# Kernel tuning notes

Measured on AMD Instinct MI355X. Metric: run time of the kernel, lower is better.

Reference implementation:

```python
import jax, jax.numpy as jnp
import numpy as np

D_MODEL = 1024
N_HEAD = 16
N_HEAD_MOE = 8
N_EXPERTS = 8
TOP_N = 2
CAP_FACTOR = 1.25
THRESHOLD = 0.2
BAL_COEF = 0.01
Z_COEF = 0.001
B, S = 8, 1024


def setup_inputs() -> dict:
    key = jax.random.key(0)
    ks = jax.random.split(key, 12)
    d, E = D_MODEL, N_EXPERTS
    w = lambda k, shape: jax.random.normal(k, shape, jnp.float32) * 0.02
    return {
        "x": jax.random.normal(ks[0], (B, S, d), jnp.float32),
        "Wq": w(ks[1], (d, d)), "Wk": w(ks[2], (d, d)), "Wv": w(ks[3], (d, d)), "Wo": w(ks[4], (d, d)),
        "bq": jnp.zeros((d,), jnp.float32), "bk": jnp.zeros((d,), jnp.float32),
        "bv": jnp.zeros((d,), jnp.float32), "bo": jnp.zeros((d,), jnp.float32),
        "ln1_g": jnp.ones((d,), jnp.float32), "ln1_b": jnp.zeros((d,), jnp.float32),
        "ln2_g": jnp.ones((d,), jnp.float32), "ln2_b": jnp.zeros((d,), jnp.float32),
        "gate_W": w(ks[5], (d, E)),
        "eWq": w(ks[6], (E, d, d)), "eWk": w(ks[7], (E, d, d)),
        "eWv": w(ks[8], (E, d, d)), "eWo": w(ks[9], (E, d, d)),
    }


def _layernorm(x, g, b, eps=1e-5):
    mu = jnp.mean(x, -1, keepdims=True)
    var = jnp.var(x, -1, keepdims=True)
    return (x - mu) * jax.lax.rsqrt(var + eps) * g + b


def _mha(x, Wq, Wk, Wv, bq, bk, bv, Wo, bo):
    b, s, d = x.shape
    h, hd = N_HEAD, d // N_HEAD
    q = (x @ Wq + bq).reshape(b, s, h, hd)
    k = (x @ Wk + bk).reshape(b, s, h, hd)
    v = (x @ Wv + bv).reshape(b, s, h, hd)
    att = jax.nn.softmax(jnp.einsum('bqhd,bkhd->bhqk', q, k) * (hd ** -0.5), axis=-1)
    o = jnp.einsum('bhqk,bkhd->bqhd', att, v).reshape(b, s, d)
    return o @ Wo + bo


def _moe(x, gate_W, eWq, eWk, eWv, eWo):
    # ST-MoE style top-n routing with capacity dropping; experts are self-attention blocks.
    b, s, d = x.shape
    E = N_EXPERTS
    C = int(S * TOP_N * CAP_FACTOR / E)  # per-expert capacity (per batch row)
    logits = x @ gate_W                      # [b,s,E]
    z_loss = jnp.mean(jnp.square(jax.nn.logsumexp(logits, axis=-1)))
    probs = jax.nn.softmax(logits, axis=-1)
    gates, idxs = jax.lax.top_k(probs, TOP_N)  # [b,s,TOP_N]
    # load-balance loss: E * sum_e (top-1 dispatch fraction) * (mean router prob)
    f = jnp.mean(jax.nn.one_hot(idxs[..., 0], E, dtype=x.dtype), axis=(0, 1))
    P = jnp.mean(probs, axis=(0, 1))
    balance_loss = E * jnp.sum(f * P)

    bb = jnp.broadcast_to(jnp.arange(b)[:, None], (b, s))
    counts = jnp.zeros((b, E), jnp.int32)
    expert_in = jnp.zeros((E, b, C, d), x.dtype)
    slots = []
    for k in range(TOP_N):  # small fixed loop over routing slots
        e_idx = idxs[..., k]
        g = gates[..., k]
        keep_thr = (g > THRESHOLD) if k > 0 else jnp.ones(g.shape, dtype=bool)
        oh = jax.nn.one_hot(e_idx, E, dtype=jnp.int32) * keep_thr[..., None].astype(jnp.int32)
        # exclusive running position within each (batch, expert) buffer
        pos_all = jnp.cumsum(oh, axis=1) - oh + counts[:, None, :]
        pos = jnp.take_along_axis(pos_all, e_idx[..., None], axis=2)[..., 0]
        counts = counts + jnp.sum(oh, axis=1)
        keep = keep_thr & (pos < C)
        p = jnp.clip(pos, 0, C - 1)
        expert_in = expert_in.at[e_idx, bb, p].add(x * keep[..., None].astype(x.dtype))
        slots.append((e_idx, p, keep, g))

    # each expert: multi-head self-attention over its C capacity slots
    h, hd = N_HEAD_MOE, d // N_HEAD_MOE
    q = jnp.einsum('ebcd,edf->ebcf', expert_in, eWq).reshape(E, b, C, h, hd)
    kk = jnp.einsum('ebcd,edf->ebcf', expert_in, eWk).reshape(E, b, C, h, hd)
    v = jnp.einsum('ebcd,edf->ebcf', expert_in, eWv).reshape(E, b, C, h, hd)
    att = jax.nn.softmax(jnp.einsum('ebqhd,ebkhd->ebhqk', q, kk) * (hd ** -0.5), axis=-1)
    o = jnp.einsum('ebhqk,ebkhd->ebqhd', att, v).reshape(E, b, C, d)
    expert_out = jnp.einsum('ebcd,edf->ebcf', o, eWo)

    # combine: gather each token's slot output, weighted by its gate
    y = jnp.zeros_like(x)
    for e_idx, p, keep, g in slots:
        y = y + expert_out[e_idx, bb, p] * (g * keep.astype(x.dtype))[..., None]
    bal = BAL_COEF * balance_loss
    zl = Z_COEF * z_loss
    return y, bal + zl, bal, zl


def reference(x, Wq, Wk, Wv, Wo, bq, bk, bv, bo, ln1_g, ln1_b, ln2_g, ln2_b,
              gate_W, eWq, eWk, eWv, eWo):
    attn = _mha(x, Wq, Wk, Wv, bq, bk, bv, Wo, bo)
    x1 = _layernorm(x + attn, ln1_g, ln1_b)
    moe_out, aux, bal, zl = _moe(x1, gate_W, eWq, eWk, eWv, eWo)
    out = _layernorm(x1 + moe_out, ln2_g, ln2_b)
    return (out, aux, bal, zl)
```

## Files before the change

### kernel.cpp

```cpp
#include <hip/hip_runtime.h>
#include <hip/hip_bf16.h>
#include <math.h>

#define DM    1024
#define NH1   16
#define HDIM1 64
#define NH2   8
#define HDIM2 128
#define NE    8
#define CAPE  320
#define BATCH 8
#define SEQ   1024
#define NTOK  (BATCH*SEQ)
#define OUTN  ((long)NTOK*DM)

typedef short bf16x8 __attribute__((ext_vector_type(8)));
typedef float f32x4  __attribute__((ext_vector_type(4)));

__device__ __forceinline__ unsigned short f2bf(float f) {
    __hip_bfloat16 h = __float2bfloat16(f);
    return *reinterpret_cast<unsigned short*>(&h);
}
__device__ __forceinline__ float bf2f(unsigned short u) {
    unsigned int x = ((unsigned int)u) << 16;
    return __builtin_bit_cast(float, x);
}

__device__ __forceinline__ void async16(const void* g, void* lds) {
    __builtin_amdgcn_global_load_lds(
        (const __attribute__((address_space(1))) unsigned int*)g,
        (__attribute__((address_space(3))) unsigned int*)lds, 16, 0, 0);
}

__device__ __forceinline__ void gemm_core(
    const unsigned short* __restrict__ A, const unsigned short* __restrict__ Bt,
    int m0, int n0, int K, short* ldsA, short* ldsB, f32x4 (&acc)[4][4])
{
    const int t    = threadIdx.x;
    const int lane = t & 63, w = t >> 6;
    const int wr = w >> 1, wc = w & 1;
    const int lq = lane >> 4, lm = lane & 15;
    const int srow = w*16 + (lane >> 2);
    const int skc  = (lane & 3) * 8;
    for (int kb = 0; kb < K; kb += 32) {
        #pragma unroll
        for (int p = 0; p < 2; ++p) {
            async16(A  + (size_t)(m0 + srow + p*64)*K + kb + skc,
                    &ldsA[(w*16 + p*64)*32]);
            async16(Bt + (size_t)(n0 + srow + p*64)*K + kb + skc,
                    &ldsB[(w*16 + p*64)*32]);
        }
        __syncthreads();
        bf16x8 aF[4], bF[4];
        #pragma unroll
        for (int i = 0; i < 4; ++i)
            aF[i] = *(const bf16x8*)&ldsA[(wr*64 + i*16 + lm)*32 + lq*8];
        #pragma unroll
        for (int j = 0; j < 4; ++j)
            bF[j] = *(const bf16x8*)&ldsB[(wc*64 + j*16 + lm)*32 + lq*8];
        #pragma unroll
        for (int i = 0; i < 4; ++i)
            #pragma unroll
            for (int j = 0; j < 4; ++j)
                acc[i][j] = __builtin_amdgcn_mfma_f32_16x16x32_bf16(aF[i], bF[j], acc[i][j], 0, 0, 0);
        __syncthreads();
    }
}

__global__ __launch_bounds__(256) void gemm_bt_f32(
    const unsigned short* __restrict__ A, const unsigned short* __restrict__ Bt,
    const float* __restrict__ bias, float* __restrict__ C, int N, int K)
{
    __shared__ short ldsA[128*32];
    __shared__ short ldsB[128*32];
    const int lane = threadIdx.x & 63, w = threadIdx.x >> 6;
    const int wr = w >> 1, wc = w & 1;
    const int lq = lane >> 4, lm = lane & 15;
    const int m0 = blockIdx.y * 128, n0 = blockIdx.x * 128;
    f32x4 acc[4][4];
    #pragma unroll
    for (int i = 0; i < 4; ++i)
        #pragma unroll
        for (int j = 0; j < 4; ++j) acc[i][j] = (f32x4){0.f,0.f,0.f,0.f};
    gemm_core(A, Bt, m0, n0, K, ldsA, ldsB, acc);
    #pragma unroll
    for (int j = 0; j < 4; ++j) {
        const int gcol = n0 + wc*64 + j*16 + lm;
        const float badd = bias ? bias[gcol] : 0.f;
        #pragma unroll
        for (int i = 0; i < 4; ++i) {
            const int grow = m0 + wr*64 + i*16 + lq*4;
            #pragma unroll
            for (int r = 0; r < 4; ++r)
                C[(size_t)(grow + r)*N + gcol] = acc[i][j][r] + badd;
        }
    }
}

__global__ __launch_bounds__(256) void gemm_qkv(
    const unsigned short* __restrict__ A, const unsigned short* __restrict__ Bt,
    const float* __restrict__ bq, const float* __restrict__ bk, const float* __restrict__ bv,
    unsigned short* __restrict__ C)
{
    __shared__ short ldsA[128*32];
    __shared__ short ldsB[128*32];
    const int lane = threadIdx.x & 63, w = threadIdx.x >> 6;
    const int wr = w >> 1, wc = w & 1;
    const int lq = lane >> 4, lm = lane & 15;
    const int m0 = blockIdx.y * 128, n0g = blockIdx.x * 128;
    const int buf = n0g >> 10;
    const float* bias = (buf == 0) ? bq : (buf == 1) ? bk : bv;
    unsigned short* Cb = C + (size_t)buf * OUTN;
    f32x4 acc[4][4];
    #pragma unroll
    for (int i = 0; i < 4; ++i)
        #pragma unroll
        for (int j = 0; j < 4; ++j) acc[i][j] = (f32x4){0.f,0.f,0.f,0.f};
    gemm_core(A, Bt, m0, n0g, DM, ldsA, ldsB, acc);
    #pragma unroll
    for (int j = 0; j < 4; ++j) {
        const int gcol = (n0g & 1023) + wc*64 + j*16 + lm;
        const float badd = bias[gcol];
        #pragma unroll
        for (int i = 0; i < 4; ++i) {
            const int grow = m0 + wr*64 + i*16 + lq*4;
            #pragma unroll
            for (int r = 0; r < 4; ++r)
                Cb[(size_t)(grow + r)*DM + gcol] = f2bf(acc[i][j][r] + badd);
        }
    }
}

__global__ __launch_bounds__(256) void gemm_eqkv_gather(
    const unsigned short* __restrict__ X1b, const int* __restrict__ slotmap,
    const unsigned short* __restrict__ zbuf,
    const unsigned short* __restrict__ eWTq, const unsigned short* __restrict__ eWTk,
    const unsigned short* __restrict__ eWTv,
    unsigned short* __restrict__ Cq, unsigned short* __restrict__ Ck,
    unsigned short* __restrict__ Cv, int ebase)
{
    __shared__ short ldsA[128*32];
    __shared__ short ldsB[128*32];
    const int lane = threadIdx.x & 63, w = threadIdx.x >> 6;
    const int wr = w >> 1, wc = w & 1;
    const int lq = lane >> 4, lm = lane & 15;
    const int z = blockIdx.z;
    const int eloc = blockIdx.y / 20;
    const unsigned short* Bt =
        ((z == 0) ? eWTq : (z == 1) ? eWTk : eWTv) + (size_t)(ebase + eloc) * (1024l*1024l);
    unsigned short* C = (z == 0) ? Cq : (z == 1) ? Ck : Cv;
    const int m0 = blockIdx.y * 128, n0 = blockIdx.x * 128;
    const int srow = w*16 + (lane >> 2);
    const int skc  = (lane & 3) * 8;
    const int sbase = ebase * (BATCH*CAPE);
    const int t0 = slotmap[sbase + m0 + srow];
    const int t1 = slotmap[sbase + m0 + srow + 64];
    const unsigned short* a0 = (t0 >= 0) ? X1b + (size_t)t0 * DM : zbuf;
    const unsigned short* a1 = (t1 >= 0) ? X1b + (size_t)t1 * DM : zbuf;
    f32x4 acc[4][4];
    #pragma unroll
    for (int i = 0; i < 4; ++i)
        #pragma unroll
        for (int j = 0; j < 4; ++j) acc[i][j] = (f32x4){0.f,0.f,0.f,0.f};
    for (int kb = 0; kb < DM; kb += 32) {
        async16(a0 + kb + skc, &ldsA[(w*16)*32]);
        async16(a1 + kb + skc, &ldsA[(w*16 + 64)*32]);
        async16(Bt + (size_t)(n0 + srow)*DM + kb + skc,      &ldsB[(w*16)*32]);
        async16(Bt + (size_t)(n0 + srow + 64)*DM + kb + skc, &ldsB[(w*16 + 64)*32]);
        __syncthreads();
        bf16x8 aF[4], bF[4];
        #pragma unroll
        for (int i = 0; i < 4; ++i)
            aF[i] = *(const bf16x8*)&ldsA[(wr*64 + i*16 + lm)*32 + lq*8];
        #pragma unroll
        for (int j = 0; j < 4; ++j)
            bF[j] = *(const bf16x8*)&ldsB[(wc*64 + j*16 + lm)*32 + lq*8];
        #pragma unroll
        for (int i = 0; i < 4; ++i)
            #pragma unroll
            for (int j = 0; j < 4; ++j)
                acc[i][j] = __builtin_amdgcn_mfma_f32_16x16x32_bf16(aF[i], bF[j], acc[i][j], 0, 0, 0);
        __syncthreads();
    }
    #pragma unroll
    for (int j = 0; j < 4; ++j) {
        const int gcol = n0 + wc*64 + j*16 + lm;
        #pragma unroll
        for (int i = 0; i < 4; ++i) {
            const int grow = m0 + wr*64 + i*16 + lq*4;
            #pragma unroll
            for (int r = 0; r < 4; ++r)
                C[(size_t)(grow + r)*DM + gcol] = f2bf(acc[i][j][r]);
        }
    }
}

__global__ __launch_bounds__(256) void gemm_eout(
    const unsigned short* __restrict__ A, const unsigned short* __restrict__ eWTo,
    unsigned short* __restrict__ C, int ebase)
{
    __shared__ short ldsA[128*32];
    __shared__ short ldsB[128*32];
    const int lane = threadIdx.x & 63, w = threadIdx.x >> 6;
    const int wr = w >> 1, wc = w & 1;
    const int lq = lane >> 4, lm = lane & 15;
    const int eloc = blockIdx.y / 20;
    const unsigned short* Bt = eWTo + (size_t)(ebase + eloc) * (1024l*1024l);
    const int m0 = blockIdx.y * 128, n0 = blockIdx.x * 128;
    f32x4 acc[4][4];
    #pragma unroll
    for (int i = 0; i < 4; ++i)
        #pragma unroll
        for (int j = 0; j < 4; ++j) acc[i][j] = (f32x4){0.f,0.f,0.f,0.f};
    gemm_core(A, Bt, m0, n0, DM, ldsA, ldsB, acc);
    #pragma unroll
    for (int j = 0; j < 4; ++j) {
        const int gcol = n0 + wc*64 + j*16 + lm;
        #pragma unroll
        for (int i = 0; i < 4; ++i) {
            const int grow = m0 + wr*64 + i*16 + lq*4;
            #pragma unroll
            for (int r = 0; r < 4; ++r)
                C[(size_t)(grow + r)*DM + gcol] = f2bf(acc[i][j][r]);
        }
    }
}

template<int HD, int NS>
__global__ __launch_bounds__(256) void flash_mfma(
    const unsigned short* __restrict__ Q, const unsigned short* __restrict__ K,
    const unsigned short* __restrict__ V, unsigned short* __restrict__ O,
    int rows, float scale)
{
    constexpr int KT = 64;
    constexpr int PADQ = HD + 8;
    constexpr int NKT = HD / 32;
    constexpr int NDT = HD / 16;
    constexpr int CG  = HD / 8;
    constexpr int RPR = 256 / CG;
    constexpr int NP  = KT / RPR;
    constexpr int PST = 76;
    __shared__ __align__(16) unsigned short ks[KT * PADQ];
    __shared__ __align__(16) unsigned short vt[HD * KT];
    __shared__ __align__(16) unsigned short pP[4][16 * PST];
    const int t = threadIdx.x, lane = t & 63, w = t >> 6;
    const int lm = lane & 15, quad = lane >> 4;
    const int q0 = blockIdx.x * (64 * NS);
    const long base = (long)blockIdx.z * rows * DM + (long)blockIdx.y * HD;
    const int srow = t / CG, scg = t % CG;

    bf16x8 aQ[NS][NKT];
    #pragma unroll
    for (int s = 0; s < NS; ++s) {
        if (s) __syncthreads();
        #pragma unroll
        for (int r = 0; r < 64 / RPR; ++r) {
            int row = srow + r * RPR;
            *(bf16x8*)&ks[row * PADQ + scg * 8] =
                *(const bf16x8*)&Q[base + (long)(q0 + s * 64 + row) * DM + scg * 8];
        }
        __syncthreads();
        #pragma unroll
        for (int kk = 0; kk < NKT; ++kk)
            aQ[s][kk] = *(const bf16x8*)&ks[(w * 16 + lm) * PADQ + kk * 32 + quad * 8];
    }

    float m4[NS][4], l4[NS][4];
    f32x4 aco[NS][NDT];
    #pragma unroll
    for (int s = 0; s < NS; ++s) {
        #pragma unroll
        for (int r = 0; r < 4; ++r) { m4[s][r] = -1e30f; l4[s][r] = 0.f; }
        #pragma unroll
        for (int d = 0; d < NDT; ++d) aco[s][d] = (f32x4){0.f,0.f,0.f,0.f};
    }

    bf16x8 kr[NP], vr[NP];
    #pragma unroll
    for (int r = 0; r < NP; ++r) {
        int row = srow + r * RPR;
        kr[r] = *(const bf16x8*)&K[base + (long)row * DM + scg * 8];
        vr[r] = *(const bf16x8*)&V[base + (long)row * DM + scg * 8];
    }

    for (int k0 = 0; k0 < rows; k0 += KT) {
        __syncthreads();
        #pragma unroll
        for (int r = 0; r < NP; ++r) {
            int row = srow + r * RPR;
            *(bf16x8*)&ks[row * PADQ + scg * 8] = kr[r];
            #pragma unroll
            for (int u = 0; u < 8; ++u) {
                int d = scg * 8 + u;
                vt[d * KT + ((((row >> 3) ^ (d >> 3) ^ d) & 7)) * 8 + (row & 7)] = ((short*)&vr[r])[u];
            }
        }
        __syncthreads();
        if (k0 + KT < rows) {
            #pragma unroll
            for (int r = 0; r < NP; ++r) {
                int row = srow + r * RPR;
                kr[r] = *(const bf16x8*)&K[base + (long)(k0 + KT + row) * DM + scg * 8];
                vr[r] = *(const bf16x8*)&V[base + (long)(k0 + KT + row) * DM + scg * 8];
            }
        }
        #pragma unroll
        for (int s = 0; s < NS; ++s) {
            f32x4 sc[4];
            #pragma unroll
            for (int n = 0; n < 4; ++n) {
                f32x4 c = (f32x4){0.f,0.f,0.f,0.f};
                #pragma unroll
                for (int kk = 0; kk < NKT; ++kk) {
                    bf16x8 bK = *(const bf16x8*)&ks[(n * 16 + lm) * PADQ + kk * 32 + quad * 8];
                    c = __builtin_amdgcn_mfma_f32_16x16x32_bf16(aQ[s][kk], bK, c, 0, 0, 0);
                }
                #pragma unroll
                for (int r = 0; r < 4; ++r) c[r] *= scale;
                sc[n] = c;
            }
            float alpha[4];
            #pragma unroll
            for (int r = 0; r < 4; ++r) {
                float mx = fmaxf(fmaxf(sc[0][r], sc[1][r]), fmaxf(sc[2][r], sc[3][r]));
                #pragma unroll
                for (int off = 1; off < 16; off <<= 1)
                    mx = fmaxf(mx, __shfl_xor(mx, off, 64));
                float mnew = fmaxf(m4[s][r], mx);
                alpha[r] = __expf(m4[s][r] - mnew);
                m4[s][r] = mnew;
                float sum = 0.f;
                #pragma unroll
                for (int n = 0; n < 4; ++n) {
                    float p = __expf(sc[n][r] - mnew);
                    sc[n][r] = p; sum += p;
                }
                #pragma unroll
                for (int off = 1; off < 16; off <<= 1)
                    sum += __shfl_xor(sum, off, 64);
                l4[s][r] = l4[s][r] * alpha[r] + sum;
            }
            #pragma unroll
            for (int n = 0; n < 4; ++n)
                #pragma unroll
                for (int r = 0; r < 4; ++r)
                    pP[w][(quad * 4 + r) * PST + n * 16 + lm] = f2bf(sc[n][r]);
            #pragma unroll
            for (int d = 0; d < NDT; ++d)
                #pragma unroll
                for (int r = 0; r < 4; ++r) aco[s][d][r] *= alpha[r];
            #pragma unroll
            for (int d = 0; d < NDT; ++d) {
                #pragma unroll
                for (int kk = 0; kk < 2; ++kk) {
                    bf16x8 aP = *(const bf16x8*)&pP[w][lm * PST + kk * 32 + quad * 8];
                    int dd = d * 16 + lm;
                    int jb = kk * 4 + quad;
                    bf16x8 bV = *(const bf16x8*)&vt[dd * KT + (((jb ^ (dd >> 3) ^ dd) & 7) * 8)];
                    aco[s][d] = __builtin_amdgcn_mfma_f32_16x16x32_bf16(aP, bV, aco[s][d], 0, 0, 0);
                }
            }
        }
    }
    #pragma unroll
    for (int s = 0; s < NS; ++s)
        #pragma unroll
        for (int r = 0; r < 4; ++r) {
            float inv = 1.f / l4[s][r];
            #pragma unroll
            for (int d = 0; d < NDT; ++d)
                O[base + (long)(q0 + s * 64 + w * 16 + quad * 4 + r) * DM + d * 16 + lm] =
                    f2bf(aco[s][d][r] * inv);
        }
}

__global__ __launch_bounds__(256) void transpose_bf16(
    const float* __restrict__ src, unsigned short* __restrict__ dst)
{
    __shared__ float tile[32][33];
    const long mb = (long)blockIdx.z * (1024l*1024l);
    const int tx = threadIdx.x & 31, ty = threadIdx.x >> 5;
    const int r0 = blockIdx.y * 32, c0 = blockIdx.x * 32;
    #pragma unroll
    for (int rr = ty; rr < 32; rr += 8)
        tile[rr][tx] = src[mb + (long)(r0+rr)*1024 + c0 + tx];
    __syncthreads();
    #pragma unroll
    for (int rr = ty; rr < 32; rr += 8)
        dst[mb + (long)(c0+rr)*1024 + r0 + tx] = f2bf(tile[tx][rr]);
}

__global__ __launch_bounds__(256) void convert_bf16(
    const float* __restrict__ src, unsigned short* __restrict__ dst, long n)
{
    long i = ((long)blockIdx.x*256 + threadIdx.x)*4;
    if (i >= n) return;
    float4 v = *(const float4*)&src[i];
    ushort4 o = { f2bf(v.x), f2bf(v.y), f2bf(v.z), f2bf(v.w) };
    *(ushort4*)&dst[i] = o;
}

__global__ __launch_bounds__(256) void ln_residual(
    const float* __restrict__ X, const float* __restrict__ R,
    const float* __restrict__ gam, const float* __restrict__ bet,
    float* __restrict__ Yf, unsigned short* __restrict__ Yb)
{
    const long row = blockIdx.x;
    const int t = threadIdx.x;
    float4 xv = *(const float4*)&X[row*DM + t*4];
    float4 rv = *(const float4*)&R[row*DM + t*4];
    float v0=xv.x+rv.x, v1=xv.y+rv.y, v2=xv.z+rv.z, v3=xv.w+rv.w;
    float s  = v0+v1+v2+v3;
    float s2 = v0*v0+v1*v1+v2*v2+v3*v3;
    #pragma unroll
    for (int off = 32; off > 0; off >>= 1) {
        s  += __shfl_down(s,  off, 64);
        s2 += __shfl_down(s2, off, 64);
    }
    __shared__ float red[8];
    __shared__ float mv[2];
    const int wid = t >> 6;
    if ((t & 63) == 0) { red[wid] = s; red[4+wid] = s2; }
    __syncthreads();
    if (t == 0) {
        float S  = red[0]+red[1]+red[2]+red[3];
        float S2 = red[4]+red[5]+red[6]+red[7];
        float mean = S * (1.f/DM);
        float var  = S2 * (1.f/DM) - mean*mean;
        mv[0] = mean; mv[1] = rsqrtf(var + 1e-5f);
    }
    __syncthreads();
    float mean = mv[0], inv = mv[1];
    float4 g4 = *(const float4*)&gam[t*4];
    float4 b4 = *(const float4*)&bet[t*4];
    float4 o4;
    o4.x = (v0-mean)*inv*g4.x + b4.x;
    o4.y = (v1-mean)*inv*g4.y + b4.y;
    o4.z = (v2-mean)*inv*g4.z + b4.z;
    o4.w = (v3-mean)*inv*g4.w + b4.w;
    *(float4*)&Yf[row*DM + t*4] = o4;
    ushort4 ub = { f2bf(o4.x), f2bf(o4.y), f2bf(o4.z), f2bf(o4.w) };
    *(ushort4*)&Yb[row*DM + t*4] = ub;
}

__global__ __launch_bounds__(256) void accum_chunk(
    float* __restrict__ out, const unsigned short* __restrict__ Eout,
    const int* __restrict__ e1, const int* __restrict__ pos1,
    const int* __restrict__ keep1, const float* __restrict__ g1,
    const int* __restrict__ e2, const int* __restrict__ pos2,
    const int* __restrict__ keep2, const float* __restrict__ g2,
    int ebase)
{
    const long row = blockIdx.x;
    const int b = (int)(row >> 10);
    const int t = threadIdx.x;
    const int E1 = e1[row] - ebase;
    const int E2 = e2[row] - ebase;
    const bool h1 = (E1 >= 0) && (E1 < 4) && (keep1[row] != 0);
    const bool h2 = (E2 >= 0) && (E2 < 4) && (keep2[row] != 0);
    if (!h1 && !h2) return;
    float4 acc = *(const float4*)&out[row*DM + t*4];
    if (h1) {
        const float w1 = g1[row];
        ushort4 u = *(const ushort4*)&Eout[((size_t)(E1*BATCH + b)*CAPE + pos1[row])*DM + t*4];
        acc.x += w1*bf2f(u.x); acc.y += w1*bf2f(u.y);
        acc.z += w1*bf2f(u.z); acc.w += w1*bf2f(u.w);
    }
    if (h2) {
        const float w2 = g2[row];
        ushort4 u = *(const ushort4*)&Eout[((size_t)(E2*BATCH + b)*CAPE + pos2[row])*DM + t*4];
        acc.x += w2*bf2f(u.x); acc.y += w2*bf2f(u.y);
        acc.z += w2*bf2f(u.z); acc.w += w2*bf2f(u.w);
    }
    *(float4*)&out[row*DM + t*4] = acc;
}

__global__ __launch_bounds__(256) void ln_inplace(
    float* __restrict__ Y, const float* __restrict__ gam, const float* __restrict__ bet)
{
    const long row = blockIdx.x;
    const int t = threadIdx.x;
    float4 xv = *(const float4*)&Y[row*DM + t*4];
    float v0=xv.x, v1=xv.y, v2=xv.z, v3=xv.w;
    float s  = v0+v1+v2+v3;
    float s2 = v0*v0+v1*v1+v2*v2+v3*v3;
    #pragma unroll
    for (int off = 32; off > 0; off >>= 1) {
        s  += __shfl_down(s,  off, 64);
        s2 += __shfl_down(s2, off, 64);
    }
    __shared__ float red[8];
    __shared__ float mv[2];
    const int wid = t >> 6;
    if ((t & 63) == 0) { red[wid] = s; red[4+wid] = s2; }
    __syncthreads();
    if (t == 0) {
        float S  = red[0]+red[1]+red[2]+red[3];
        float S2 = red[4]+red[5]+red[6]+red[7];
        float mean = S * (1.f/DM);
        float var  = S2 * (1.f/DM) - mean*mean;
        mv[0] = mean; mv[1] = rsqrtf(var + 1e-5f);
    }
    __syncthreads();
    float mean = mv[0], inv = mv[1];
    float4 g4 = *(const float4*)&gam[t*4];
    float4 b4 = *(const float4*)&bet[t*4];
    float4 o4;
    o4.x = (v0-mean)*inv*g4.x + b4.x;
    o4.y = (v1-mean)*inv*g4.y + b4.y;
    o4.z = (v2-mean)*inv*g4.z + b4.z;
    o4.w = (v3-mean)*inv*g4.w + b4.w;
    *(float4*)&Y[row*DM + t*4] = o4;
}

__global__ __launch_bounds__(256) void gate_kernel(
    const float* __restrict__ X1, const float* __restrict__ gW,
    int* __restrict__ e1, int* __restrict__ e2,
    float* __restrict__ g1, float* __restrict__ g2,
    float* __restrict__ accum)
{
    const int t = threadIdx.x, l = t & 63, w = t >> 6;
    const int gwave = blockIdx.x * 4 + w;
    float zacc = 0.f, pacc[8], facc[8];
    #pragma unroll
    for (int e = 0; e < 8; ++e) { pacc[e] = 0.f; facc[e] = 0.f; }

    for (int tok = gwave; tok < NTOK; tok += 2048) {
        const float* xr = X1 + (long)tok*DM;
        float part[8];
        #pragma unroll
        for (int e = 0; e < 8; ++e) part[e] = 0.f;
        #pragma unroll
        for (int pass = 0; pass < 4; ++pass) {
            const int i0 = pass*256 + l*4;
            float4 xv = *(const float4*)&xr[i0];
            const float xs[4] = {xv.x, xv.y, xv.z, xv.w};
            #pragma unroll
            for (int u = 0; u < 4; ++u) {
                float4 w0 = *(const float4*)&gW[(i0+u)*8];
                float4 w1 = *(const float4*)&gW[(i0+u)*8+4];
                part[0]+=xs[u]*w0.x; part[1]+=xs[u]*w0.y; part[2]+=xs[u]*w0.z; part[3]+=xs[u]*w0.w;
                part[4]+=xs[u]*w1.x; part[5]+=xs[u]*w1.y; part[6]+=xs[u]*w1.z; part[7]+=xs[u]*w1.w;
            }
        }
        #pragma unroll
        for (int e = 0; e < 8; ++e) {
            float v = part[e];
            #pragma unroll
            for (int off = 32; off > 0; off >>= 1) v += __shfl_down(v, off, 64);
            part[e] = v;
        }
        if (l == 0) {
            float mx = part[0];
            #pragma unroll
            for (int e = 1; e < 8; ++e) mx = fmaxf(mx, part[e]);
            float p[8]; float sum = 0.f;
            #pragma unroll
            for (int e = 0; e < 8; ++e) { p[e] = __expf(part[e]-mx); sum += p[e]; }
            float lse = mx + __logf(sum);
            float isum = 1.f/sum;
            #pragma unroll
            for (int e = 0; e < 8; ++e) { p[e] *= isum; pacc[e] += p[e]; }
            int b1 = 0;
            #pragma unroll
            for (int e = 1; e < 8; ++e) if (p[e] > p[b1]) b1 = e;
            int b2 = (b1 == 0) ? 1 : 0;
            #pragma unroll
            for (int e = 0; e < 8; ++e) if (e != b1 && e != b2 && p[e] > p[b2]) b2 = e;
            e1[tok] = b1; e2[tok] = b2; g1[tok] = p[b1]; g2[tok] = p[b2];
            zacc += lse*lse;
            facc[b1] += 1.f;
        }
    }
    __shared__ float red[4][17];
    if (l == 0) {
        red[w][0] = zacc;
        #pragma unroll
        for (int e = 0; e < 8; ++e) { red[w][1+e] = pacc[e]; red[w][9+e] = facc[e]; }
    }
    __syncthreads();
    if (t < 17)
        atomicAdd(&accum[t], red[0][t] + red[1][t] + red[2][t] + red[3][t]);
}

__global__ __launch_bounds__(64) void route_scan(
    const int* __restrict__ e1, const int* __restrict__ e2,
    const float* __restrict__ g2,
    int* __restrict__ pos1, int* __restrict__ keep1,
    int* __restrict__ pos2, int* __restrict__ keep2,
    int* __restrict__ slotmap)
{
    const int b = blockIdx.x;
    const int l = threadIdx.x;
    __shared__ int cnt[8];
    if (l < 8) cnt[l] = 0;
    __syncthreads();
    for (int slot = 0; slot < 2; ++slot) {
        const int* eArr = slot ? e2 : e1;
        for (int c = 0; c < SEQ/64; ++c) {
            const int tk = b*SEQ + c*64 + l;
            const int e = eArr[tk];
            const bool valid = slot ? (g2[tk] > 0.2f) : true;
            unsigned long long mymask = 0ull; int addmine = 0;
            #pragma unroll
            for (int ee = 0; ee < 8; ++ee) {
                unsigned long long bm = __ballot(valid && (e == ee));
                if (e == ee) mymask = bm;
                if (l == ee) addmine = (int)__popcll(bm);
            }
            const int p  = cnt[e] + (int)__popcll(mymask & ((1ull << l) - 1ull));
            const int kp = (valid && p < CAPE) ? 1 : 0;
            const int pc = p < CAPE ? p : (CAPE-1);
            if (slot == 0) { pos1[tk] = pc; keep1[tk] = kp; }
            else           { pos2[tk] = pc; keep2[tk] = kp; }
            if (kp) slotmap[(e*BATCH + b)*CAPE + pc] = tk;
            __syncthreads();
            if (l < 8) cnt[l] += addmine;
            __syncthreads();
        }
    }
}

__global__ void finalize_loss(const float* __restrict__ accum, float* __restrict__ out)
{
    float z = accum[0] * (1.0f/NTOK);
    float s = 0.f;
    for (int e = 0; e < 8; ++e)
        s += (accum[1+e] * (1.0f/NTOK)) * (accum[9+e] * (1.0f/NTOK));
    float bal = 0.01f * 8.0f * s;
    float zl  = 0.001f * z;
    out[OUTN]   = bal + zl;
    out[OUTN+1] = bal;
    out[OUTN+2] = zl;
}

extern "C" void kernel_launch(void* const* d_in, const int* in_sizes, int n_in,
                              void* d_out, int out_size, void* d_ws, size_t ws_size,
                              hipStream_t stream)
{
    (void)in_sizes; (void)n_in; (void)out_size; (void)ws_size;
    const float* x    = (const float*)d_in[0];
    const float* Wq   = (const float*)d_in[1];
    const float* Wk   = (const float*)d_in[2];
    const float* Wv   = (const float*)d_in[3];
    const float* Wo   = (const float*)d_in[4];
    const float* bq   = (const float*)d_in[5];
    const float* bk   = (const float*)d_in[6];
    const float* bv   = (const float*)d_in[7];
    const float* bo   = (const float*)d_in[8];
    const float* ln1g = (const float*)d_in[9];
    const float* ln1b = (const float*)d_in[10];
    const float* ln2g = (const float*)d_in[11];
    const float* ln2b = (const float*)d_in[12];
    const float* gW   = (const float*)d_in[13];
    const float* eWq  = (const float*)d_in[14];
    const float* eWk  = (const float*)d_in[15];
    const float* eWv  = (const float*)d_in[16];
    const float* eWo  = (const float*)d_in[17];
    float* out = (float*)d_out;

    char* ws = (char*)d_ws;
    const size_t MB = 1048576;
    const long MATE = 1024l*1024l;
    unsigned short* WTq  = (unsigned short*)(ws);
    unsigned short* WTk  = WTq + 1*MATE;
    unsigned short* WTv  = WTq + 2*MATE;
    unsigned short* WTo  = WTq + 3*MATE;
    unsigned short* eWTq = WTq + 4*MATE;
    unsigned short* eWTk = WTq + 12*MATE;
    unsigned short* eWTv = WTq + 20*MATE;
    unsigned short* eWTo = WTq + 28*MATE;
    int*   e1i   = (int*)(ws + 72*MB);
    int*   e2i   = e1i + NTOK;
    int*   pos1  = e1i + 2*NTOK;
    int*   pos2  = e1i + 3*NTOK;
    int*   keep1 = e1i + 4*NTOK;
    int*   keep2 = e1i + 5*NTOK;
    int*   slotmap = e1i + 6*NTOK;
    float* g1f   = (float*)(e1i + 6*NTOK + NE*BATCH*CAPE);
    float* g2f   = g1f + NTOK;
    float* accum = g2f + NTOK;
    unsigned short* zbuf = (unsigned short*)(ws + 73*MB);
    unsigned short* xb  = (unsigned short*)(ws + 74*MB);
    unsigned short* x1b = (unsigned short*)(ws + 74*MB);
    unsigned short* ob  = (unsigned short*)(ws + 90*MB);
    unsigned short* Qb  = (unsigned short*)(ws + 106*MB);
    float* Pf = (float*)(ws + 106*MB);
    unsigned short* eqb = (unsigned short*)(ws + 90*MB);
    unsigned short* ekb = (unsigned short*)(ws + 110*MB);
    unsigned short* evb = (unsigned short*)(ws + 130*MB);
    unsigned short* eob = (unsigned short*)(ws + 150*MB);
    unsigned short* eoc = eqb;

    dim3 blk(256);
    dim3 tgrid(32, 32, 1), tgrid8(32, 32, 8);

    transpose_bf16<<<tgrid,  blk, 0, stream>>>(Wq,  WTq);
    transpose_bf16<<<tgrid,  blk, 0, stream>>>(Wk,  WTk);
    transpose_bf16<<<tgrid,  blk, 0, stream>>>(Wv,  WTv);
    transpose_bf16<<<tgrid,  blk, 0, stream>>>(Wo,  WTo);
    transpose_bf16<<<tgrid8, blk, 0, stream>>>(eWq, eWTq);
    transpose_bf16<<<tgrid8, blk, 0, stream>>>(eWk, eWTk);
    transpose_bf16<<<tgrid8, blk, 0, stream>>>(eWv, eWTv);
    transpose_bf16<<<tgrid8, blk, 0, stream>>>(eWo, eWTo);
    convert_bf16<<<NTOK, blk, 0, stream>>>(x, xb, OUTN);

    gemm_qkv<<<dim3(3*DM/128, NTOK/128), blk, 0, stream>>>(xb, WTq, bq, bk, bv, Qb);
    flash_mfma<HDIM1,1><<<dim3(SEQ/64, NH1, BATCH), blk, 0, stream>>>(
        Qb, Qb + OUTN, Qb + 2*OUTN, ob, SEQ, 0.125f);
    gemm_bt_f32<<<dim3(DM/128, NTOK/128), blk, 0, stream>>>(ob, WTo, bo, Pf, DM, DM);
    ln_residual<<<NTOK, blk, 0, stream>>>(x, Pf, ln1g, ln1b, out, x1b);

    hipMemsetAsync(accum, 0, 17*sizeof(float), stream);
    hipMemsetAsync(slotmap, 0xFF, NE*BATCH*CAPE*sizeof(int), stream);
    hipMemsetAsync(zbuf, 0, 4096, stream);
    gate_kernel<<<512, blk, 0, stream>>>(out, gW, e1i, e2i, g1f, g2f, accum);
    route_scan<<<BATCH, dim3(64), 0, stream>>>(e1i, e2i, g2f, pos1, keep1, pos2, keep2, slotmap);

    for (int c = 0; c < 2; ++c) {
        const int ebase = c*4;
        gemm_eqkv_gather<<<dim3(DM/128, 4*BATCH*CAPE/128, 3), blk, 0, stream>>>(
            x1b, slotmap, zbuf, eWTq, eWTk, eWTv, eqb, ekb, evb, ebase);
        flash_mfma<HDIM2,1><<<dim3(CAPE/64, NH2, 4*BATCH), blk, 0, stream>>>(
            eqb, ekb, evb, eob, CAPE, 0.088388347648318447f);
        gemm_eout<<<dim3(DM/128, 4*BATCH*CAPE/128), blk, 0, stream>>>(
            eob, eWTo, eoc, ebase);
        accum_chunk<<<NTOK, blk, 0, stream>>>(out, eoc, e1i, pos1, keep1, g1f,
                                              e2i, pos2, keep2, g2f, ebase);
    }

    ln_inplace<<<NTOK, blk, 0, stream>>>(out, ln2g, ln2b);
    finalize_loss<<<1, 1, 0, stream>>>(accum, out);
}
```

Before: 917.0 us.

## Add lazy softmax rescale, batch weight transposes, and process all experts per chunk

The flash attention loop now skips the exp-rescale of the running max and the accumulator unless some row's new max exceeds the old one by more than 8, which saves exp and multiply work on most tiles. The eight weight-transpose launches are merged into two. When the workspace is large enough, all eight experts are processed in one chunk instead of two, halving the launches of the expert kernels and the accumulation pass. The lazy rescale lets probabilities exceed 1 (up to e^8) before bf16 rounding, and the chunk size now depends on the workspace size.

New measurement: 935.4 us. +2.0%, slower.

```diff
diff --git a/kernel.cpp b/kernel.cpp
--- a/kernel.cpp
+++ b/kernel.cpp
@@ -319,36 +319,56 @@
                 for (int r = 0; r < 4; ++r) c[r] *= scale;
                 sc[n] = c;
             }
-            float alpha[4];
+            float mxv[4];
+            bool need = false;
             #pragma unroll
             for (int r = 0; r < 4; ++r) {
                 float mx = fmaxf(fmaxf(sc[0][r], sc[1][r]), fmaxf(sc[2][r], sc[3][r]));
                 #pragma unroll
                 for (int off = 1; off < 16; off <<= 1)
                     mx = fmaxf(mx, __shfl_xor(mx, off, 64));
-                float mnew = fmaxf(m4[s][r], mx);
-                alpha[r] = __expf(m4[s][r] - mnew);
-                m4[s][r] = mnew;
-                float sum = 0.f;
+                mxv[r] = mx;
+                need = need || (mx > m4[s][r] + 8.f);
+            }
+            if (__any(need ? 1 : 0)) {
                 #pragma unroll
-                for (int n = 0; n < 4; ++n) {
-                    float p = __expf(sc[n][r] - mnew);
-                    sc[n][r] = p; sum += p;
+                for (int r = 0; r < 4; ++r) {
+                    float mnew = fmaxf(m4[s][r], mxv[r]);
+                    float alpha = __expf(m4[s][r] - mnew);
+                    m4[s][r] = mnew;
+                    float sum = 0.f;
+                    #pragma unroll
+                    for (int n = 0; n < 4; ++n) {
+                        float p = __expf(sc[n][r] - mnew);
+                        sc[n][r] = p; sum += p;
+                    }
+                    #pragma unroll
+                    for (int off = 1; off < 16; off <<= 1)
+                        sum += __shfl_xor(sum, off, 64);
+                    l4[s][r] = l4[s][r] * alpha + sum;
+                    #pragma unroll
+                    for (int d = 0; d < NDT; ++d) aco[s][d][r] *= alpha;
                 }
+            } else {
                 #pragma unroll
-                for (int off = 1; off < 16; off <<= 1)
-                    sum += __shfl_xor(sum, off, 64);
-                l4[s][r] = l4[s][r] * alpha[r] + sum;
+                for (int r = 0; r < 4; ++r) {
+                    float sum = 0.f;
+                    #pragma unroll
+                    for (int n = 0; n < 4; ++n) {
+                        float p = __expf(sc[n][r] - m4[s][r]);
+                        sc[n][r] = p; sum += p;
+                    }
+                    #pragma unroll
+                    for (int off = 1; off < 16; off <<= 1)
+                        sum += __shfl_xor(sum, off, 64);
+                    l4[s][r] += sum;
+                }
             }
             #pragma unroll
             for (int n = 0; n < 4; ++n)
                 #pragma unroll
                 for (int r = 0; r < 4; ++r)
                     pP[w][(quad * 4 + r) * PST + n * 16 + lm] = f2bf(sc[n][r]);
-            #pragma unroll
-            for (int d = 0; d < NDT; ++d)
-                #pragma unroll
-                for (int r = 0; r < 4; ++r) aco[s][d][r] *= alpha[r];
             #pragma unroll
             for (int d = 0; d < NDT; ++d) {
                 #pragma unroll
@@ -374,20 +394,26 @@
         }
 }
 
-__global__ __launch_bounds__(256) void transpose_bf16(
-    const float* __restrict__ src, unsigned short* __restrict__ dst)
+__global__ __launch_bounds__(256) void transpose_many(
+    const float* __restrict__ s0, const float* __restrict__ s1,
+    const float* __restrict__ s2, const float* __restrict__ s3,
+    unsigned short* __restrict__ dst, int per)
 {
     __shared__ float tile[32][33];
-    const long mb = (long)blockIdx.z * (1024l*1024l);
+    const int z = blockIdx.z;
+    const int m = z / per;
+    const float* src = ((m == 0) ? s0 : (m == 1) ? s1 : (m == 2) ? s2 : s3)
+                       + (long)(z % per) * (1024l*1024l);
+    unsigned short* d = dst + (long)z * (1024l*1024l);
     const int tx = threadIdx.x & 31, ty = threadIdx.x >> 5;
     const int r0 = blockIdx.y * 32, c0 = blockIdx.x * 32;
     #pragma unroll
     for (int rr = ty; rr < 32; rr += 8)
-        tile[rr][tx] = src[mb + (long)(r0+rr)*1024 + c0 + tx];
+        tile[rr][tx] = src[(long)(r0+rr)*1024 + c0 + tx];
     __syncthreads();
     #pragma unroll
     for (int rr = ty; rr < 32; rr += 8)
-        dst[mb + (long)(c0+rr)*1024 + r0 + tx] = f2bf(tile[tx][rr]);
+        d[(long)(c0+rr)*1024 + r0 + tx] = f2bf(tile[tx][rr]);
 }
 
 __global__ __launch_bounds__(256) void convert_bf16(
@@ -449,15 +475,15 @@
     const int* __restrict__ keep1, const float* __restrict__ g1,
     const int* __restrict__ e2, const int* __restrict__ pos2,
     const int* __restrict__ keep2, const float* __restrict__ g2,
-    int ebase)
+    int ebase, int epc)
 {
     const long row = blockIdx.x;
     const int b = (int)(row >> 10);
     const int t = threadIdx.x;
     const int E1 = e1[row] - ebase;
     const int E2 = e2[row] - ebase;
-    const bool h1 = (E1 >= 0) && (E1 < 4) && (keep1[row] != 0);
-    const bool h2 = (E2 >= 0) && (E2 < 4) && (keep2[row] != 0);
+    const bool h1 = (E1 >= 0) && (E1 < epc) && (keep1[row] != 0);
+    const bool h2 = (E2 >= 0) && (E2 < epc) && (keep2[row] != 0);
     if (!h1 && !h2) return;
     float4 acc = *(const float4*)&out[row*DM + t*4];
     if (h1) {
@@ -638,7 +664,7 @@
                               void* d_out, int out_size, void* d_ws, size_t ws_size,
                               hipStream_t stream)
 {
-    (void)in_sizes; (void)n_in; (void)out_size; (void)ws_size;
+    (void)in_sizes; (void)n_in; (void)out_size;
     const float* x    = (const float*)d_in[0];
     const float* Wq   = (const float*)d_in[1];
     const float* Wk   = (const float*)d_in[2];
@@ -663,13 +689,11 @@
     const size_t MB = 1048576;
     const long MATE = 1024l*1024l;
     unsigned short* WTq  = (unsigned short*)(ws);
-    unsigned short* WTk  = WTq + 1*MATE;
-    unsigned short* WTv  = WTq + 2*MATE;
-    unsigned short* WTo  = WTq + 3*MATE;
     unsigned short* eWTq = WTq + 4*MATE;
     unsigned short* eWTk = WTq + 12*MATE;
     unsigned short* eWTv = WTq + 20*MATE;
     unsigned short* eWTo = WTq + 28*MATE;
+    unsigned short* WTo  = WTq + 3*MATE;
     int*   e1i   = (int*)(ws + 72*MB);
     int*   e2i   = e1i + NTOK;
     int*   pos1  = e1i + 2*NTOK;
@@ -686,23 +710,18 @@
     unsigned short* ob  = (unsigned short*)(ws + 90*MB);
     unsigned short* Qb  = (unsigned short*)(ws + 106*MB);
     float* Pf = (float*)(ws + 106*MB);
+    const int epc = (ws_size >= (size_t)250*MB) ? 8 : 4;
+    const long ebuf = (long)epc * BATCH * CAPE * DM;
     unsigned short* eqb = (unsigned short*)(ws + 90*MB);
-    unsigned short* ekb = (unsigned short*)(ws + 110*MB);
-    unsigned short* evb = (unsigned short*)(ws + 130*MB);
-    unsigned short* eob = (unsigned short*)(ws + 150*MB);
+    unsigned short* ekb = eqb + ebuf;
+    unsigned short* evb = ekb + ebuf;
+    unsigned short* eob = evb + ebuf;
     unsigned short* eoc = eqb;
 
     dim3 blk(256);
-    dim3 tgrid(32, 32, 1), tgrid8(32, 32, 8);
-
-    transpose_bf16<<<tgrid,  blk, 0, stream>>>(Wq,  WTq);
-    transpose_bf16<<<tgrid,  blk, 0, stream>>>(Wk,  WTk);
-    transpose_bf16<<<tgrid,  blk, 0, stream>>>(Wv,  WTv);
-    transpose_bf16<<<tgrid,  blk, 0, stream>>>(Wo,  WTo);
-    transpose_bf16<<<tgrid8, blk, 0, stream>>>(eWq, eWTq);
-    transpose_bf16<<<tgrid8, blk, 0, stream>>>(eWk, eWTk);
-    transpose_bf16<<<tgrid8, blk, 0, stream>>>(eWv, eWTv);
-    transpose_bf16<<<tgrid8, blk, 0, stream>>>(eWo, eWTo);
+
+    transpose_many<<<dim3(32, 32, 4),  blk, 0, stream>>>(Wq, Wk, Wv, Wo, WTq, 1);
+    transpose_many<<<dim3(32, 32, 32), blk, 0, stream>>>(eWq, eWk, eWv, eWo, eWTq, 8);
     convert_bf16<<<NTOK, blk, 0, stream>>>(x, xb, OUTN);
 
     gemm_qkv<<<dim3(3*DM/128, NTOK/128), blk, 0, stream>>>(xb, WTq, bq, bk, bv, Qb);
@@ -717,16 +736,16 @@
     gate_kernel<<<512, blk, 0, stream>>>(out, gW, e1i, e2i, g1f, g2f, accum);
     route_scan<<<BATCH, dim3(64), 0, stream>>>(e1i, e2i, g2f, pos1, keep1, pos2, keep2, slotmap);
 
-    for (int c = 0; c < 2; ++c) {
-        const int ebase = c*4;
-        gemm_eqkv_gather<<<dim3(DM/128, 4*BATCH*CAPE/128, 3), blk, 0, stream>>>(
+    for (int c = 0; c < 8/epc; ++c) {
+        const int ebase = c*epc;
+        gemm_eqkv_gather<<<dim3(DM/128, epc*20, 3), blk, 0, stream>>>(
             x1b, slotmap, zbuf, eWTq, eWTk, eWTv, eqb, ekb, evb, ebase);
-        flash_mfma<HDIM2,1><<<dim3(CAPE/64, NH2, 4*BATCH), blk, 0, stream>>>(
+        flash_mfma<HDIM2,1><<<dim3(CAPE/64, NH2, epc*BATCH), blk, 0, stream>>>(
             eqb, ekb, evb, eob, CAPE, 0.088388347648318447f);
-        gemm_eout<<<dim3(DM/128, 4*BATCH*CAPE/128), blk, 0, stream>>>(
+        gemm_eout<<<dim3(DM/128, epc*20), blk, 0, stream>>>(
             eob, eWTo, eoc, ebase);
         accum_chunk<<<NTOK, blk, 0, stream>>>(out, eoc, e1i, pos1, keep1, g1f,
-                                              e2i, pos2, keep2, g2f, ebase);
+                                              e2i, pos2, keep2, g2f, ebase, epc);
     }
 
     ln_inplace<<<NTOK, blk, 0, stream>>>(out, ln2g, ln2b);
```
